# Kernel tuning notes

Measured on AMD Instinct MI355X. Metric: run time of the kernel, lower is better.

Reference implementation:

```python
import jax, jax.numpy as jnp
import numpy as np
import math

C_S = 384; C_Z = 128; C_H = 16; H = 12; PQ = 4; PV = 8; C_SURF = 16
N_RES = 512; N_SURF = 2048; B = 1
INF = 1e5; EPS = 1e-8
SOFTPLUS_INV_1 = 0.541324854612918


def _quat_to_rot(q):
    q = q / jnp.linalg.norm(q, axis=-1, keepdims=True)
    w, x, y, z = q[..., 0], q[..., 1], q[..., 2], q[..., 3]
    R = jnp.stack([
        1 - 2 * (y * y + z * z), 2 * (x * y - w * z), 2 * (x * z + w * y),
        2 * (x * y + w * z), 1 - 2 * (x * x + z * z), 2 * (y * z - w * x),
        2 * (x * z - w * y), 2 * (y * z + w * x), 1 - 2 * (x * x + y * y),
    ], axis=-1)
    return R.reshape(q.shape[:-1] + (3, 3))


def setup_inputs() -> dict:
    key = jax.random.key(0)
    ks = jax.random.split(key, 32)
    hc = H * C_H            # 192
    hpq = H * PQ * 3        # 144
    hpkv = H * (PQ + PV) * 3  # 432
    cz4 = C_Z // 4
    concat = hc + H * PV * 3 + H * PV + H * cz4 + hc  # 1152
    w = lambda k, i, o: jax.random.normal(k, (i, o), jnp.float32) * 0.02
    inp = {
        's': jax.random.normal(ks[0], (B, N_RES, C_S), jnp.float32),
        'z': jax.random.normal(ks[1], (B, N_RES, N_RES, C_Z), jnp.float32),
        'rots': _quat_to_rot(jax.random.normal(ks[2], (B, N_RES, 4), jnp.float32)),
        'trans': jax.random.normal(ks[3], (B, N_RES, 3), jnp.float32) * 10.0,
        'mask': jnp.ones((B, N_RES), jnp.float32),
        'surface_points': jax.random.normal(ks[4], (B, N_SURF, 3), jnp.float32) * 10.0,
        'surface_features': jax.random.normal(ks[5], (B, N_SURF, C_SURF), jnp.float32),
        'surface_mask': jnp.ones((B, N_SURF), jnp.float32),
        'Wq': w(ks[6], C_S, hc), 'bq': jnp.zeros((hc,)),
        'Wkv': w(ks[7], C_S, 2 * hc), 'bkv': jnp.zeros((2 * hc,)),
        'Wqp': w(ks[8], C_S, hpq), 'bqp': jnp.zeros((hpq,)),
        'Wkvp': w(ks[9], C_S, hpkv), 'bkvp': jnp.zeros((hpkv,)),
        'Wse': w(ks[10], C_SURF, C_S), 'bse': jnp.zeros((C_S,)),
        'Wsq': w(ks[11], C_S, hc), 'bsq': jnp.zeros((hc,)),
        'Wsk': w(ks[12], C_S, hc), 'bsk': jnp.zeros((hc,)),
        'Wsv': w(ks[13], C_S, hc), 'bsv': jnp.zeros((hc,)),
        'Wb': w(ks[14], C_Z, H), 'bb': jnp.zeros((H,)),
        'Wdz': w(ks[15], C_Z, cz4), 'bdz': jnp.zeros((cz4,)),
        'head_weights': jnp.full((H,), SOFTPLUS_INV_1, jnp.float32),
        'sb_weights': jnp.full((1,), SOFTPLUS_INV_1, jnp.float32),
        'Wout': w(ks[16], concat, C_S), 'bout': jnp.zeros((C_S,)),
        'Wso': w(ks[17], 2 * C_S, C_SURF), 'bso': jnp.zeros((C_SURF,)),
    }
    return inp


def reference(s, z, rots, trans, mask, surface_points, surface_features, surface_mask,
              Wq, bq, Wkv, bkv, Wqp, bqp, Wkvp, bkvp, Wse, bse, Wsq, bsq, Wsk, bsk,
              Wsv, bsv, Wb, bb, Wdz, bdz, head_weights, sb_weights, Wout, bout, Wso, bso):
    lin = lambda x, W, b: x @ W + b
    b_, n, _ = s.shape
    m = surface_points.shape[-2]

    surface_feat = lin(surface_features, Wse, bse)                    # [B,M,c_s]
    # backbone<->surface squared distances
    disp = trans[:, :, None, :] - surface_points[:, None, :, :]       # [B,N,M,3]
    dist_sq = jnp.sum(disp * disp, -1)                                # [B,N,M]

    q = lin(s, Wq, bq).reshape(b_, n, H, C_H)
    kv = lin(s, Wkv, bkv).reshape(b_, n, H, 2 * C_H)
    k, v = kv[..., :C_H], kv[..., C_H:]

    # query points: split into 3 coord chunks, stack, rigid-apply
    qp = lin(s, Wqp, bqp)
    qp = jnp.stack(jnp.split(qp, 3, axis=-1), axis=-1)                # [B,N,H*PQ,3]
    qp = jnp.einsum('bnij,bnpj->bnpi', rots, qp) + trans[:, :, None]
    qp = qp.reshape(b_, n, H, PQ, 3)

    kvp = lin(s, Wkvp, bkvp)
    kvp = jnp.stack(jnp.split(kvp, 3, axis=-1), axis=-1)              # [B,N,H*(PQ+PV),3]
    kvp = jnp.einsum('bnij,bnpj->bnpi', rots, kvp) + trans[:, :, None]
    kvp = kvp.reshape(b_, n, H, PQ + PV, 3)
    kp, vp = kvp[..., :PQ, :], kvp[..., PQ:, :]

    b_bias = lin(z, Wb, bb)                                           # [B,N,N,H]
    a = jnp.einsum('bihc,bjhc->bhij', q, k) * math.sqrt(1.0 / (3 * C_H))
    a = a + math.sqrt(1.0 / 3) * jnp.transpose(b_bias, (0, 3, 1, 2))

    # point-distance attention term
    pt = jnp.sum((qp[:, :, None] - kp[:, None]) ** 2, axis=-1)        # [B,N,N,H,PQ]
    hw = jax.nn.softplus(head_weights)                                # [H]
    pt = jnp.sum(pt, axis=-1) * hw * math.sqrt(1.0 / (3 * (PQ * 9.0 / 2))) * (-0.5)
    a = a + jnp.transpose(pt, (0, 3, 1, 2))                           # [B,H,N,N]

    sq_mask = INF * (mask[:, :, None] * mask[:, None, :] - 1.0)
    a = jax.nn.softmax(a + sq_mask[:, None], axis=-1)

    o = jnp.einsum('bhij,bjhc->bihc', a, v).reshape(b_, n, H * C_H)
    o_pt = jnp.einsum('bhij,bjhpd->bihpd', a, vp)                     # [B,N,H,PV,3]
    o_pt = jnp.einsum('bnji,bnhpj->bnhpi', rots, o_pt - trans[:, :, None, None])
    o_pt_norm = jnp.sqrt(jnp.sum(o_pt ** 2, -1) + EPS).reshape(b_, n, H * PV)
    o_pt_flat = o_pt.reshape(b_, n, H * PV, 3)

    pair_z = lin(z, Wdz, bdz)                                         # [B,N,N,cz/4]
    o_pair = jnp.einsum('bhij,bijc->bihc', a, pair_z).reshape(b_, n, -1)

    # surface cross-attention branch
    sq = lin(s, Wsq, bsq).reshape(b_, n, H, C_H)
    sk = lin(surface_feat, Wsk, bsk).reshape(b_, m, H, C_H)
    sv = lin(surface_feat, Wsv, bsv).reshape(b_, m, H, C_H)
    logits = jnp.einsum('bnhc,bmhc->bhnm', sq, sk) * math.sqrt(1.0 / C_H)
    sbw = jax.nn.softplus(sb_weights)[0]
    logits = logits - 0.5 * sbw * dist_sq[:, None]
    cross_mask = mask[:, :, None] * surface_mask[:, None, :]          # [B,N,M]
    logits = logits + INF * (cross_mask - 1.0)[:, None]
    a_s = jax.nn.softmax(logits, axis=-1)
    o_surf = jnp.einsum('bhnm,bmhc->bnhc', a_s, sv).reshape(b_, n, H * C_H)

    o_cat = jnp.concatenate([o, o_pt_flat[..., 0], o_pt_flat[..., 1], o_pt_flat[..., 2],
                             o_pt_norm, o_pair, o_surf], axis=-1)
    s_out = lin(o_cat, Wout, bout)                                    # [B,N,c_s]

    # surface update: attend surface points to backbone (softmax over residues)
    a_ts = jax.nn.softmax(jnp.swapaxes(logits, -1, -2), axis=-1).mean(axis=1)  # [B,M,N]
    s_agg = jnp.einsum('bmn,bnc->bmc', a_ts, s)
    surf_out = lin(jnp.concatenate([surface_feat, s_agg], axis=-1), Wso, bso)
    return s_out, surf_out
```

## Files before the change

### kernel.cpp

```cpp
#include <hip/hip_runtime.h>
#include <cstddef>


#define CS 384
#define INFV 100000.0f

__device__ __forceinline__ float softplusf(float x) { return log1pf(__expf(x)); }

__global__ __launch_bounds__(256) void k_pack(
    const float* __restrict__ Wq, const float* __restrict__ Wsq,
    const float* __restrict__ Wkv, const float* __restrict__ Wqp,
    const float* __restrict__ Wkvp, const float* __restrict__ Wsk,
    const float* __restrict__ Wsv, const float* __restrict__ Wout,
    const float* __restrict__ bq, const float* __restrict__ bsq,
    const float* __restrict__ bkv, const float* __restrict__ bqp,
    const float* __restrict__ bkvp, const float* __restrict__ bsk,
    const float* __restrict__ bsv,
    float* __restrict__ wt1, float* __restrict__ wt2, float* __restrict__ wt3,
    float* __restrict__ b1, float* __restrict__ b2)
{
    const int b = blockIdx.x, t = threadIdx.x;
    if (b >= 1092) {
        int idx = (b - 1092) * 256 + t;
        if (idx < 1344) {
            float v;
            if (idx < 192) v = bq[idx];
            else if (idx < 384) v = bsq[idx - 192];
            else if (idx < 768) v = bkv[idx - 384];
            else if (idx < 912) v = bqp[idx - 768];
            else v = bkvp[idx - 912];
            b1[idx] = v;
        } else if (idx < 1728) {
            int i2 = idx - 1344;
            b2[i2] = (i2 < 192) ? bsk[i2] : bsv[i2 - 192];
        }
        return;
    }
    const float* src; float* dst; int C, coff, tile, ldd;
    if (b < 72)       { src = Wq;   C = 192; dst = wt1; coff = 0;   ldd = 384;  tile = b; }
    else if (b < 144) { src = Wsq;  C = 192; dst = wt1; coff = 192; ldd = 384;  tile = b - 72; }
    else if (b < 288) { src = Wkv;  C = 384; dst = wt1; coff = 384; ldd = 384;  tile = b - 144; }
    else if (b < 348) { src = Wqp;  C = 144; dst = wt1; coff = 768; ldd = 384;  tile = b - 288; }
    else if (b < 516) { src = Wkvp; C = 432; dst = wt1; coff = 912; ldd = 384;  tile = b - 348; }
    else if (b < 588) { src = Wsk;  C = 192; dst = wt2; coff = 0;   ldd = 384;  tile = b - 516; }
    else if (b < 660) { src = Wsv;  C = 192; dst = wt2; coff = 192; ldd = 384;  tile = b - 588; }
    else              { src = Wout; C = 384; dst = wt3; coff = 0;   ldd = 1152; tile = b - 660; }
    const int cT = (C + 31) >> 5;
    const int tk = tile / cT, tc = tile % cT;
    __shared__ float l[32][33];
    const int tr = t >> 5, tcc = t & 31;
    #pragma unroll
    for (int rr = 0; rr < 4; ++rr) {
        int kloc = tr * 4 + rr;
        int cg = tc * 32 + tcc;
        l[kloc][tcc] = (cg < C) ? src[(size_t)(tk * 32 + kloc) * C + cg] : 0.f;
    }
    __syncthreads();
    #pragma unroll
    for (int rr = 0; rr < 4; ++rr) {
        int cloc = tr * 4 + rr;
        int cg = tc * 32 + cloc;
        if (cg < C) dst[(size_t)(coff + cg) * ldd + tk * 32 + tcc] = l[tcc][cloc];
    }
}

__global__ __launch_bounds__(256) void k_packz(
    const float* __restrict__ Wb, const float* __restrict__ bb,
    const float* __restrict__ Wdz, const float* __restrict__ bdz,
    float* __restrict__ wz, float* __restrict__ bz)
{
    const float s3 = 0.5773502691896258f;
    int idx = blockIdx.x * 256 + threadIdx.x;
    if (idx < 5632) {
        int c = idx >> 7, kk = idx & 127;
        wz[idx] = (c < 12) ? s3 * Wb[kk * 12 + c] : Wdz[kk * 32 + (c - 12)];
    } else if (idx < 5676) {
        int c = idx - 5632;
        bz[c] = (c < 12) ? s3 * bb[c] : bdz[c - 12];
    }
}

__global__ __launch_bounds__(256) void k_transp(
    const float* __restrict__ A, float* __restrict__ At)
{
    __shared__ float tile[32][33];
    const int r0 = blockIdx.y * 32, c0 = blockIdx.x * 32;
    const int tr = threadIdx.x >> 5, tc = threadIdx.x & 31;
    #pragma unroll
    for (int rr = 0; rr < 4; ++rr)
        tile[tr + rr * 8][tc] = A[(size_t)(r0 + tr + rr * 8) * 384 + c0 + tc];
    __syncthreads();
    #pragma unroll
    for (int rr = 0; rr < 4; ++rr)
        At[(size_t)(c0 + tr + rr * 8) * 512 + r0 + tc] = tile[tc][tr + rr * 8];
}

template<int KTOT, bool HB>
__global__ __launch_bounds__(256) void k_gemm(
    const float* __restrict__ A, const float* __restrict__ Wt,
    const float* __restrict__ bias, float* __restrict__ C, int ldc)
{
    __shared__ float As[64][68];
    __shared__ float Ws[64][68];
    const int t = threadIdx.x;
    const int c0 = blockIdx.x * 64, m0 = blockIdx.y * 64;
    const int sr = t >> 4, sk4 = (t & 15) << 2;
    const int wid = t >> 6, lane = t & 63;
    const int wr = (wid >> 1) * 32, wc = (wid & 1) * 32;
    const int lr = lane >> 3, lc = lane & 7;
    float acc[4][4];
    #pragma unroll
    for (int j = 0; j < 4; ++j) {
        float bv = HB ? bias[c0 + wc + lc + 8 * j] : 0.f;
        #pragma unroll
        for (int i = 0; i < 4; ++i) acc[i][j] = bv;
    }
    for (int kc = 0; kc < KTOT; kc += 64) {
        __syncthreads();
        #pragma unroll
        for (int rep = 0; rep < 4; ++rep) {
            int row = sr + rep * 16;
            *(float4*)&As[row][sk4] = *(const float4*)&A[(size_t)(m0 + row) * KTOT + kc + sk4];
            *(float4*)&Ws[row][sk4] = *(const float4*)&Wt[(size_t)(c0 + row) * KTOT + kc + sk4];
        }
        __syncthreads();
        #pragma unroll 4
        for (int k4 = 0; k4 < 16; ++k4) {
            float4 a[4], w[4];
            #pragma unroll
            for (int i = 0; i < 4; ++i) a[i] = *(float4*)&As[wr + lr + 8 * i][k4 * 4];
            #pragma unroll
            for (int j = 0; j < 4; ++j) w[j] = *(float4*)&Ws[wc + lc + 8 * j][k4 * 4];
            #pragma unroll
            for (int i = 0; i < 4; ++i) {
                #pragma unroll
                for (int j = 0; j < 4; ++j) {
                    acc[i][j] = fmaf(a[i].x, w[j].x, acc[i][j]);
                    acc[i][j] = fmaf(a[i].y, w[j].y, acc[i][j]);
                    acc[i][j] = fmaf(a[i].z, w[j].z, acc[i][j]);
                    acc[i][j] = fmaf(a[i].w, w[j].w, acc[i][j]);
                }
            }
        }
    }
    #pragma unroll
    for (int i = 0; i < 4; ++i) {
        #pragma unroll
        for (int j = 0; j < 4; ++j)
            C[(size_t)(m0 + wr + lr + 8 * i) * ldc + c0 + wc + lc + 8 * j] = acc[i][j];
    }
}

__global__ __launch_bounds__(256) void k_scatter(
    const float* __restrict__ proj, const float* __restrict__ rots,
    const float* __restrict__ trans,
    float* __restrict__ qw, float* __restrict__ kw, float* __restrict__ vw,
    float* __restrict__ sqw, float* __restrict__ qpw, float* __restrict__ kpw,
    float* __restrict__ vpw)
{
    __shared__ float p[4][1344];
    const int n0 = blockIdx.x * 4, t = threadIdx.x;
    for (int idx = t; idx < 1344; idx += 256) {
        #pragma unroll
        for (int r = 0; r < 4; ++r) p[r][idx] = proj[(size_t)(n0 + r) * 1344 + idx];
    }
    __syncthreads();
    for (int idx = t; idx < 3072; idx += 256) {
        int r = idx / 768, c = idx % 768;
        int n = n0 + r;
        float v = p[r][c];
        if (c < 192) qw[(size_t)n * 192 + c] = v;
        else if (c < 384) sqw[(size_t)n * 192 + (c - 192)] = v;
        else {
            int cc = c - 384, h = cc >> 5, sub = cc & 31;
            if (sub < 16) kw[(size_t)n * 192 + h * 16 + sub] = v;
            else          vw[(size_t)n * 192 + h * 16 + (sub - 16)] = v;
        }
    }
    for (int idx = t; idx < 2304; idx += 256) {
        int r = idx / 576, rem = idx % 576;
        int n = n0 + r;
        const float* R = &rots[(size_t)n * 9];
        const float* tr = &trans[(size_t)n * 3];
        if (rem < 144) {
            int pp = rem / 3, d = rem % 3;
            float v = fmaf(R[d*3+0], p[r][768 + pp],
                      fmaf(R[d*3+1], p[r][768 + 48 + pp],
                      fmaf(R[d*3+2], p[r][768 + 96 + pp], tr[d])));
            qpw[(size_t)n * 144 + pp * 3 + d] = v;
        } else {
            int rem2 = rem - 144; int pp = rem2 / 3, d = rem2 % 3;
            float v = fmaf(R[d*3+0], p[r][912 + pp],
                      fmaf(R[d*3+1], p[r][912 + 144 + pp],
                      fmaf(R[d*3+2], p[r][912 + 288 + pp], tr[d])));
            int h = pp / 12, ii = pp % 12;
            if (ii < 4) kpw[(size_t)n * 144 + h * 12 + ii * 3 + d] = v;
            else        vpw[(size_t)n * 288 + h * 24 + (ii - 4) * 3 + d] = v;
        }
    }
}

__global__ __launch_bounds__(256) void k_sfeat(
    const float* __restrict__ sf, const float* __restrict__ Wse,
    const float* __restrict__ bse, float* __restrict__ sfeat)
{
    __shared__ float wl[16 * 384];
    __shared__ float sfl[8][16];
    const int m0 = blockIdx.x * 8, t = threadIdx.x;
    for (int idx = t; idx < 6144; idx += 256) wl[idx] = Wse[idx];
    if (t < 128) sfl[t >> 4][t & 15] = sf[(size_t)(m0 + (t >> 4)) * 16 + (t & 15)];
    __syncthreads();
    #pragma unroll
    for (int u = 0; u < 12; ++u) {
        int idx = t + u * 256;
        int r = idx / 384, c = idx % 384;
        float a = bse[c];
        #pragma unroll
        for (int kk = 0; kk < 16; ++kk) a = fmaf(sfl[r][kk], wl[kk * 384 + c], a);
        sfeat[(size_t)(m0 + r) * 384 + c] = a;
    }
}

__global__ __launch_bounds__(256) void k_zpass(
    const float* __restrict__ z, const float* __restrict__ wz,
    const float* __restrict__ bz, float* __restrict__ bpz)
{
    __shared__ float zt[256][36];
    __shared__ float wt[44][32];
    const int t = threadIdx.x;
    const int jg0 = blockIdx.x * 256;
    const int i = jg0 >> 9;
    const int jloc = jg0 & 511;
    const int jl = t & 63;
    const int cgs = __builtin_amdgcn_readfirstlane(t >> 6);
    float acc[4][11];
    #pragma unroll
    for (int u = 0; u < 11; ++u) {
        float b = bz[cgs * 11 + u];
        acc[0][u] = b; acc[1][u] = b; acc[2][u] = b; acc[3][u] = b;
    }
    for (int kc = 0; kc < 128; kc += 32) {
        __syncthreads();
        for (int idx = t; idx < 352; idx += 256) {
            int c = idx >> 3, k4 = (idx & 7) << 2;
            *(float4*)&wt[c][k4] = *(const float4*)&wz[c * 128 + kc + k4];
        }
        #pragma unroll
        for (int u = 0; u < 8; ++u) {
            int idx = t + u * 256;
            int r = idx >> 3, k4 = (idx & 7) << 2;
            *(float4*)&zt[r][k4] = *(const float4*)&z[((size_t)(jg0 + r)) * 128 + kc + k4];
        }
        __syncthreads();
        const float* wbase = &wt[cgs * 11][0];
        #pragma unroll 2
        for (int k4 = 0; k4 < 32; k4 += 4) {
            float4 z0 = *(float4*)&zt[jl][k4];
            float4 z1 = *(float4*)&zt[jl + 64][k4];
            float4 z2 = *(float4*)&zt[jl + 128][k4];
            float4 z3 = *(float4*)&zt[jl + 192][k4];
            #pragma unroll
            for (int u = 0; u < 11; ++u) {
                float4 wv = *(const float4*)&wbase[u * 32 + k4];
                acc[0][u] = fmaf(z0.x, wv.x, fmaf(z0.y, wv.y,
                            fmaf(z0.z, wv.z, fmaf(z0.w, wv.w, acc[0][u]))));
                acc[1][u] = fmaf(z1.x, wv.x, fmaf(z1.y, wv.y,
                            fmaf(z1.z, wv.z, fmaf(z1.w, wv.w, acc[1][u]))));
                acc[2][u] = fmaf(z2.x, wv.x, fmaf(z2.y, wv.y,
                            fmaf(z2.z, wv.z, fmaf(z2.w, wv.w, acc[2][u]))));
                acc[3][u] = fmaf(z3.x, wv.x, fmaf(z3.y, wv.y,
                            fmaf(z3.z, wv.z, fmaf(z3.w, wv.w, acc[3][u]))));
            }
        }
    }
    #pragma unroll
    for (int u = 0; u < 11; ++u) {
        size_t base = ((size_t)i * 44 + cgs * 11 + u) * 512 + jloc;
        bpz[base + jl]       = acc[0][u];
        bpz[base + 64 + jl]  = acc[1][u];
        bpz[base + 128 + jl] = acc[2][u];
        bpz[base + 192 + jl] = acc[3][u];
    }
}

__global__ __launch_bounds__(256) void k_attn_a(
    const float* __restrict__ qw, const float* __restrict__ kw,
    const float* __restrict__ qpw, const float* __restrict__ kpw,
    const float* __restrict__ bpz, const float* __restrict__ mask,
    const float* __restrict__ hwp, float* __restrict__ abuf)
{
    __shared__ float pls[4][520];
    __shared__ float qs[64], qps[48], cpt4[4];
    const int i = blockIdx.x, hg = blockIdx.y;
    const int t = threadIdx.x;
    if (t < 64) qs[t] = qw[(size_t)i * 192 + hg * 64 + t];
    if (t < 48) qps[t] = qpw[(size_t)i * 144 + hg * 48 + t];
    if (t < 4) cpt4[t] = -0.5f * 0.13608276348795434f * softplusf(hwp[hg * 4 + t]);
    const float mask_i = mask[i];
    __syncthreads();
    #pragma unroll 2
    for (int it = 0; it < 8; ++it) {
        int idx = t + it * 256;
        int hh = idx >> 9, j = idx & 511;
        int h = hg * 4 + hh;
        float kj[16], kpj[12];
        { const float4* kr = (const float4*)&kw[(size_t)j * 192 + h * 16];
          *(float4*)&kj[0] = kr[0]; *(float4*)&kj[4] = kr[1];
          *(float4*)&kj[8] = kr[2]; *(float4*)&kj[12] = kr[3]; }
        { const float4* kr = (const float4*)&kpw[(size_t)j * 144 + h * 12];
          *(float4*)&kpj[0] = kr[0]; *(float4*)&kpj[4] = kr[1]; *(float4*)&kpj[8] = kr[2]; }
        float qk = 0.f;
        #pragma unroll
        for (int c = 0; c < 16; ++c) qk = fmaf(qs[hh * 16 + c], kj[c], qk);
        float pts = 0.f;
        #pragma unroll
        for (int p = 0; p < 4; ++p) {
            float dx = qps[hh*12+p*3+0] - kpj[p*3+0];
            float dy = qps[hh*12+p*3+1] - kpj[p*3+1];
            float dz = qps[hh*12+p*3+2] - kpj[p*3+2];
            pts += dx*dx + dy*dy + dz*dz;
        }
        float lg = fmaf(0.14433756729740643f, qk, bpz[((size_t)i * 44 + h) * 512 + j]);
        lg = fmaf(cpt4[hh], pts, lg);
        lg += INFV * (mask_i * mask[j] - 1.0f);
        pls[hh][j] = lg;
    }
    __syncthreads();
    const int w = t >> 6, lane = t & 63;
    float v[8];
    #pragma unroll
    for (int k = 0; k < 8; ++k) v[k] = pls[w][lane + k * 64];
    float mx = v[0];
    #pragma unroll
    for (int k = 1; k < 8; ++k) mx = fmaxf(mx, v[k]);
    #pragma unroll
    for (int off = 32; off; off >>= 1) mx = fmaxf(mx, __shfl_xor(mx, off));
    float sm = 0.f;
    #pragma unroll
    for (int k = 0; k < 8; ++k) { v[k] = __expf(v[k] - mx); sm += v[k]; }
    #pragma unroll
    for (int off = 32; off; off >>= 1) sm += __shfl_xor(sm, off);
    const float inv = 1.0f / sm;
    float* dst = abuf + ((size_t)(hg * 4 + w) * 512 + i) * 512;
    #pragma unroll
    for (int k = 0; k < 8; ++k) dst[lane + k * 64] = v[k] * inv;
}

__global__ __launch_bounds__(256) void k_attn_pair(
    const float* __restrict__ abuf, const float* __restrict__ bpz,
    float* __restrict__ ocat)
{
    __shared__ float al[12][512];
    const int i = blockIdx.x, t = threadIdx.x;
    #pragma unroll
    for (int u = 0; u < 12; ++u) {
        al[u][t] = abuf[(size_t)u * 262144 + (size_t)i * 512 + t];
        al[u][t + 256] = abuf[(size_t)u * 262144 + (size_t)i * 512 + t + 256];
    }
    __syncthreads();
    const int c = t & 31;
    const int h1 = t >> 5;
    const bool dual = (t < 128);
    const float* pz = bpz + ((size_t)i * 44 + 12 + c) * 512;
    const float* a1 = al[h1];
    const float* a2 = al[dual ? h1 + 8 : 0];
    float acc1 = 0.f, acc2 = 0.f;
    for (int j = 0; j < 512; j += 4) {
        float4 p = *(const float4*)&pz[j];
        acc1 = fmaf(a1[j+0], p.x, acc1);
        acc1 = fmaf(a1[j+1], p.y, acc1);
        acc1 = fmaf(a1[j+2], p.z, acc1);
        acc1 = fmaf(a1[j+3], p.w, acc1);
        if (dual) {
            acc2 = fmaf(a2[j+0], p.x, acc2);
            acc2 = fmaf(a2[j+1], p.y, acc2);
            acc2 = fmaf(a2[j+2], p.z, acc2);
            acc2 = fmaf(a2[j+3], p.w, acc2);
        }
    }
    ocat[(size_t)i * 1152 + 576 + h1 * 32 + c] = acc1;
    if (dual) ocat[(size_t)i * 1152 + 576 + (h1 + 8) * 32 + c] = acc2;
}

__global__ __launch_bounds__(256) void k_gemm_ov(
    const float* __restrict__ abuf, const float* __restrict__ vw,
    const float* __restrict__ vpw, float* __restrict__ cbuf)
{
    __shared__ float As[64][68];
    __shared__ float Bs[64][44];
    const int i0 = blockIdx.x * 64, h = blockIdx.y;
    const int t = threadIdx.x;
    const int sr = t >> 4, sk4 = (t & 15) << 2;
    const int r1 = t >> 3;
    const int cb = t & 7;
    float acc[2][5];
    #pragma unroll
    for (int u = 0; u < 5; ++u) { acc[0][u] = 0.f; acc[1][u] = 0.f; }
    for (int kc = 0; kc < 512; kc += 64) {
        __syncthreads();
        #pragma unroll
        for (int rep = 0; rep < 4; ++rep) {
            int row = sr + rep * 16;
            *(float4*)&As[row][sk4] =
                *(const float4*)&abuf[(size_t)h * 262144 + (size_t)(i0 + row) * 512 + kc + sk4];
        }
        #pragma unroll
        for (int u = 0; u < 10; ++u) {
            int idx = t + u * 256;
            int r = idx / 40, cc = idx % 40;
            Bs[r][cc] = (cc < 16) ? vw[(size_t)(kc + r) * 192 + h * 16 + cc]
                                  : vpw[(size_t)(kc + r) * 288 + h * 24 + (cc - 16)];
        }
        __syncthreads();
        #pragma unroll 4
        for (int kk = 0; kk < 64; ++kk) {
            float av1 = As[r1][kk], av2 = As[r1 + 32][kk];
            #pragma unroll
            for (int u = 0; u < 5; ++u) {
                float b = Bs[kk][cb + 8 * u];
                acc[0][u] = fmaf(av1, b, acc[0][u]);
                acc[1][u] = fmaf(av2, b, acc[1][u]);
            }
        }
    }
    #pragma unroll
    for (int u = 0; u < 5; ++u) {
        cbuf[((size_t)h * 512 + i0 + r1) * 40 + cb + 8 * u] = acc[0][u];
        cbuf[((size_t)h * 512 + i0 + r1 + 32) * 40 + cb + 8 * u] = acc[1][u];
    }
}

__global__ __launch_bounds__(256) void k_optfin(
    const float* __restrict__ cbuf, const float* __restrict__ rots,
    const float* __restrict__ trans, float* __restrict__ ocat)
{
    __shared__ float cl[4][12][40];
    const int i0 = blockIdx.x * 4, t = threadIdx.x;
    for (int idx = t; idx < 1920; idx += 256) {
        int ii = idx / 480, rem = idx % 480;
        int h = rem / 40, c = rem % 40;
        cl[ii][h][c] = cbuf[((size_t)h * 512 + i0 + ii) * 40 + c];
    }
    __syncthreads();
    for (int idx = t; idx < 768; idx += 256) {
        int ii = idx / 192, o = idx % 192;
        ocat[(size_t)(i0 + ii) * 1152 + o] = cl[ii][o >> 4][o & 15];
    }
    for (int idx = t; idx < 384; idx += 256) {
        int ii = idx / 96, hp = idx % 96;
        int h = hp >> 3, p = hp & 7;
        int i = i0 + ii;
        const float* R = &rots[(size_t)i * 9];
        float gx = cl[ii][h][16 + p*3 + 0] - trans[(size_t)i*3 + 0];
        float gy = cl[ii][h][16 + p*3 + 1] - trans[(size_t)i*3 + 1];
        float gz = cl[ii][h][16 + p*3 + 2] - trans[(size_t)i*3 + 2];
        float lx = R[0]*gx + R[3]*gy + R[6]*gz;
        float ly = R[1]*gx + R[4]*gy + R[7]*gz;
        float lz = R[2]*gx + R[5]*gy + R[8]*gz;
        float nm = sqrtf(lx*lx + ly*ly + lz*lz + 1e-8f);
        int col = h * 8 + p;
        size_t base = (size_t)i * 1152;
        ocat[base + 192 + col] = lx;
        ocat[base + 288 + col] = ly;
        ocat[base + 384 + col] = lz;
        ocat[base + 480 + col] = nm;
    }
}

__global__ __launch_bounds__(256) void k_tlog(
    const float* __restrict__ sqw, const float* __restrict__ skv,
    const float* __restrict__ trans, const float* __restrict__ mask,
    const float* __restrict__ sp, const float* __restrict__ smask,
    const float* __restrict__ sbwp, float* __restrict__ logits,
    float* __restrict__ stat_m, float* __restrict__ stat_il)
{
    __shared__ float sk_s[32][16];
    __shared__ float sq_s[32][16];
    __shared__ float trans_s[96];
    __shared__ float mask_s[32];
    __shared__ float spm_s[96];
    __shared__ float smask_s[32];
    const int h = blockIdx.y;
    const int m0 = blockIdx.x * 32;
    const int t = threadIdx.x;
    const int tmg = t >> 5, tnl = t & 31;
    const float sbw = softplusf(sbwp[0]);
    for (int idx = t; idx < 512; idx += 256) {
        int row = idx >> 4, c = idx & 15;
        sk_s[row][c] = skv[(size_t)(m0 + row) * 384 + h * 16 + c];
    }
    if (t < 96) spm_s[t] = sp[(size_t)m0 * 3 + t];
    if (t < 32) smask_s[t] = smask[m0 + t];
    __syncthreads();
    float skr[4][16];
    float spx[4], spy[4], spz[4], smk[4];
    #pragma unroll
    for (int mi = 0; mi < 4; ++mi) {
        int row = tmg * 4 + mi;
        #pragma unroll
        for (int c4 = 0; c4 < 16; c4 += 4)
            *(float4*)&skr[mi][c4] = *(float4*)&sk_s[row][c4];
        spx[mi] = spm_s[row*3+0]; spy[mi] = spm_s[row*3+1]; spz[mi] = spm_s[row*3+2];
        smk[mi] = smask_s[row];
    }
    float mxr[4], lr[4];
    #pragma unroll
    for (int mi = 0; mi < 4; ++mi) { mxr[mi] = -1e30f; lr[mi] = 0.f; }
    for (int nt = 0; nt < 16; ++nt) {
        __syncthreads();
        const int nb = nt * 32;
        if (t < 128) {
            int nn = t >> 2, c4 = (t & 3) << 2;
            *(float4*)&sq_s[nn][c4] = *(const float4*)&sqw[(size_t)(nb + nn) * 192 + h * 16 + c4];
        }
        if (t < 96) trans_s[t] = trans[(size_t)nb * 3 + t];
        if (t < 32) mask_s[t] = mask[nb + t];
        __syncthreads();
        float q[16];
        #pragma unroll
        for (int c4 = 0; c4 < 16; c4 += 4)
            *(float4*)&q[c4] = *(float4*)&sq_s[tnl][c4];
        const float tx = trans_s[tnl*3+0], ty = trans_s[tnl*3+1], tz = trans_s[tnl*3+2];
        const float mkn = mask_s[tnl];
        #pragma unroll
        for (int mi = 0; mi < 4; ++mi) {
            float dot = 0.f;
            #pragma unroll
            for (int c = 0; c < 16; ++c) dot = fmaf(skr[mi][c], q[c], dot);
            float dx = tx - spx[mi], dy = ty - spy[mi], dz = tz - spz[mi];
            float mterm = INFV * (mkn * smk[mi] - 1.0f) - 0.5f * sbw * (dx*dx + dy*dy + dz*dz);
            float lg = fmaf(0.25f, dot, mterm);
            logits[((size_t)(m0 + tmg * 4 + mi) * 12 + h) * 512 + nb + tnl] = lg;
            float newm = fmaxf(mxr[mi], lg);
            lr[mi] = lr[mi] * __expf(mxr[mi] - newm) + __expf(lg - newm);
            mxr[mi] = newm;
        }
    }
    #pragma unroll
    for (int off = 1; off < 32; off <<= 1) {
        #pragma unroll
        for (int mi = 0; mi < 4; ++mi) {
            float m2 = __shfl_xor(mxr[mi], off), l2 = __shfl_xor(lr[mi], off);
            float newm = fmaxf(mxr[mi], m2);
            lr[mi] = lr[mi] * __expf(mxr[mi] - newm) + l2 * __expf(m2 - newm);
            mxr[mi] = newm;
        }
    }
    if (tnl == 0) {
        #pragma unroll
        for (int mi = 0; mi < 4; ++mi) {
            int m = m0 + tmg * 4 + mi;
            stat_m[(size_t)m * 12 + h] = mxr[mi];
            stat_il[(size_t)m * 12 + h] = 1.0f / lr[mi];
        }
    }
}

__global__ __launch_bounds__(256) void k_rstat(
    const float* __restrict__ lbuf, float* __restrict__ rspm,
    float* __restrict__ rsps)
{
    __shared__ float smx[4][64], ssm[4][64];
    const int n0 = blockIdx.x * 64, mc = blockIdx.y, h = blockIdx.z;
    const int t = threadIdx.x, ln = t & 63, mg = t >> 6;
    const int mb = mc * 512;
    const int n = n0 + ln;
    float mx = -1e30f, sm = 0.f;
    #pragma unroll 2
    for (int it = 0; it < 128; ++it) {
        int m = mb + it * 4 + mg;
        float lg = lbuf[((size_t)m * 12 + h) * 512 + n];
        float nm = fmaxf(mx, lg);
        sm = sm * __expf(mx - nm) + __expf(lg - nm);
        mx = nm;
    }
    smx[mg][ln] = mx; ssm[mg][ln] = sm;
    __syncthreads();
    if (t < 64) {
        float M = smx[0][t], S = ssm[0][t];
        #pragma unroll
        for (int g = 1; g < 4; ++g) {
            float m2 = smx[g][t], s2 = ssm[g][t];
            float nm = fmaxf(M, m2);
            S = S * __expf(M - nm) + s2 * __expf(m2 - nm);
            M = nm;
        }
        rspm[((size_t)h * 4 + mc) * 512 + n0 + t] = M;
        rsps[((size_t)h * 4 + mc) * 512 + n0 + t] = S;
    }
}

__global__ __launch_bounds__(256) void k_rcomb(
    const float* __restrict__ rspm, const float* __restrict__ rsps,
    float* __restrict__ rmax, float* __restrict__ rinv)
{
    int gid = blockIdx.x * 256 + threadIdx.x;
    if (gid >= 6144) return;
    int h = gid >> 9, n = gid & 511;
    float M = -1e30f, S = 0.f;
    #pragma unroll
    for (int mc = 0; mc < 4; ++mc) {
        float m2 = rspm[((size_t)h * 4 + mc) * 512 + n];
        float s2 = rsps[((size_t)h * 4 + mc) * 512 + n];
        float nm = fmaxf(M, m2);
        S = S * __expf(M - nm) + s2 * __expf(m2 - nm);
        M = nm;
    }
    rmax[gid] = M;
    rinv[gid] = 1.0f / S;
}

__global__ __launch_bounds__(256) void k_pv(
    const float* __restrict__ lbuf, const float* __restrict__ skv,
    const float* __restrict__ rmax, const float* __restrict__ rinv,
    float* __restrict__ pvp)
{
    __shared__ float sv_s[512][17];
    const int n0 = blockIdx.x * 64, mc = blockIdx.y, h = blockIdx.z;
    const int t = threadIdx.x, ln = t & 63, mg = t >> 6;
    const int mb = mc * 512;
    for (int idx = t; idx < 2048; idx += 256) {
        int ml = idx >> 2, c4 = (idx & 3) << 2;
        float4 v4 = *(const float4*)&skv[(size_t)(mb + ml) * 384 + 192 + h * 16 + c4];
        sv_s[ml][c4+0]=v4.x; sv_s[ml][c4+1]=v4.y; sv_s[ml][c4+2]=v4.z; sv_s[ml][c4+3]=v4.w;
    }
    const int n = n0 + ln;
    const float rm = rmax[h * 512 + n], ri = rinv[h * 512 + n];
    float acc[16];
    #pragma unroll
    for (int c = 0; c < 16; ++c) acc[c] = 0.f;
    __syncthreads();
    #pragma unroll 2
    for (int it = 0; it < 128; ++it) {
        int ml = it * 4 + mg;
        float w = __expf(lbuf[((size_t)(mb + ml) * 12 + h) * 512 + n] - rm) * ri;
        #pragma unroll
        for (int c = 0; c < 16; ++c) acc[c] = fmaf(w, sv_s[ml][c], acc[c]);
    }
    __syncthreads();
    float* red = &sv_s[0][0];
    #pragma unroll
    for (int c = 0; c < 16; ++c) red[(mg * 64 + ln) * 17 + c] = acc[c];
    __syncthreads();
    {
        int nl = t >> 2, c4 = (t & 3) << 2;
        float4 o;
        #pragma unroll
        for (int e = 0; e < 4; ++e) {
            float s = 0.f;
            #pragma unroll
            for (int g = 0; g < 4; ++g) s += red[(g * 64 + nl) * 17 + c4 + e];
            (&o.x)[e] = s;
        }
        *(float4*)&pvp[(((size_t)h * 4 + mc) * 512 + n0 + nl) * 16 + c4] = o;
    }
}

__global__ __launch_bounds__(256) void k_pvcomb(
    const float* __restrict__ pvp, float* __restrict__ ocat)
{
    int gid = blockIdx.x * 256 + threadIdx.x;
    int n = gid / 192, rem = gid % 192;
    float o = 0.f;
    #pragma unroll
    for (int mc = 0; mc < 4; ++mc)
        o += pvp[(((size_t)(rem >> 4) * 4 + mc) * 512 + n) * 16 + (rem & 15)];
    ocat[(size_t)n * 1152 + 960 + rem] = o;
}

__global__ __launch_bounds__(256) void k_tw(
    const float* __restrict__ logits, const float* __restrict__ stat_m,
    const float* __restrict__ stat_il, float* __restrict__ w)
{
    __shared__ float mxs[12], ils[12];
    const int m = blockIdx.x, t = threadIdx.x;
    if (t < 12) { mxs[t] = stat_m[(size_t)m * 12 + t]; ils[t] = stat_il[(size_t)m * 12 + t]; }
    __syncthreads();
    const float* lp = logits + (size_t)m * 12 * 512;
    float a0 = 0.f, a1 = 0.f;
    #pragma unroll
    for (int h = 0; h < 12; ++h) {
        a0 += __expf(lp[h * 512 + t] - mxs[h]) * ils[h];
        a1 += __expf(lp[h * 512 + 256 + t] - mxs[h]) * ils[h];
    }
    w[(size_t)m * 512 + t] = a0 * (1.0f / 12.0f);
    w[(size_t)m * 512 + 256 + t] = a1 * (1.0f / 12.0f);
}

__global__ __launch_bounds__(256) void k_surf_out(
    const float* __restrict__ sfeat, const float* __restrict__ saggw,
    const float* __restrict__ Wso, const float* __restrict__ bso,
    float* __restrict__ out)
{
    __shared__ float wl[12304];
    const int t = threadIdx.x;
    for (int idx = t; idx < 12288; idx += 256) {
        int k = idx >> 4, c = idx & 15;
        wl[(k / 192) * 3076 + (k % 192) * 16 + c] = Wso[idx];
    }
    const int m = blockIdx.x * 64 + (t >> 2);
    const int kq = t & 3;
    const float* src = (kq < 2) ? &sfeat[(size_t)m * 384 + kq * 192]
                                : &saggw[(size_t)m * 384 + (kq - 2) * 192];
    __syncthreads();
    float acc[16];
    #pragma unroll
    for (int c = 0; c < 16; ++c) acc[c] = 0.f;
    const float* wb = &wl[kq * 3076];
    for (int k = 0; k < 192; k += 4) {
        float4 v = *(const float4*)&src[k];
        #pragma unroll
        for (int e = 0; e < 4; ++e) {
            float sv = (&v.x)[e];
            #pragma unroll
            for (int c = 0; c < 16; ++c)
                acc[c] = fmaf(sv, wb[(k + e) * 16 + c], acc[c]);
        }
    }
    #pragma unroll
    for (int c = 0; c < 16; ++c) {
        acc[c] += __shfl_xor(acc[c], 1);
        acc[c] += __shfl_xor(acc[c], 2);
    }
    #pragma unroll
    for (int c = 0; c < 16; ++c) {
        if ((c >> 2) == kq) out[196608 + (size_t)m * 16 + c] = acc[c] + bso[c];
    }
}

extern "C" void kernel_launch(void* const* d_in, const int* in_sizes, int n_in,
                              void* d_out, int out_size, void* d_ws, size_t ws_size,
                              hipStream_t stream)
{
    (void)in_sizes; (void)n_in; (void)out_size; (void)ws_size;
    const float* s     = (const float*)d_in[0];
    const float* z     = (const float*)d_in[1];
    const float* rots  = (const float*)d_in[2];
    const float* trans = (const float*)d_in[3];
    const float* mask  = (const float*)d_in[4];
    const float* sp    = (const float*)d_in[5];
    const float* sf    = (const float*)d_in[6];
    const float* smask = (const float*)d_in[7];
    const float* Wq    = (const float*)d_in[8];  const float* bq   = (const float*)d_in[9];
    const float* Wkv   = (const float*)d_in[10]; const float* bkv  = (const float*)d_in[11];
    const float* Wqp   = (const float*)d_in[12]; const float* bqp  = (const float*)d_in[13];
    const float* Wkvp  = (const float*)d_in[14]; const float* bkvp = (const float*)d_in[15];
    const float* Wse   = (const float*)d_in[16]; const float* bse  = (const float*)d_in[17];
    const float* Wsq   = (const float*)d_in[18]; const float* bsq  = (const float*)d_in[19];
    const float* Wsk   = (const float*)d_in[20]; const float* bsk  = (const float*)d_in[21];
    const float* Wsv   = (const float*)d_in[22]; const float* bsv  = (const float*)d_in[23];
    const float* Wb    = (const float*)d_in[24]; const float* bb   = (const float*)d_in[25];
    const float* Wdz   = (const float*)d_in[26]; const float* bdz  = (const float*)d_in[27];
    const float* hw    = (const float*)d_in[28]; const float* sbw  = (const float*)d_in[29];
    const float* Wout  = (const float*)d_in[30]; const float* bout = (const float*)d_in[31];
    const float* Wso   = (const float*)d_in[32]; const float* bso  = (const float*)d_in[33];
    float* out = (float*)d_out;

    float* qw    = (float*)d_ws;
    float* kw    = qw    + (size_t)512 * 192;
    float* vw    = kw    + (size_t)512 * 192;
    float* sqw   = vw    + (size_t)512 * 192;
    float* qpw   = sqw   + (size_t)512 * 192;
    float* kpw   = qpw   + (size_t)512 * 144;
    float* vpw   = kpw   + (size_t)512 * 144;
    float* sfeat = vpw   + (size_t)512 * 288;
    float* skv   = sfeat + (size_t)2048 * 384;
    float* ocat  = skv   + (size_t)2048 * 384;
    float* sagg  = ocat  + (size_t)512 * 1152;
    float* region = sagg + (size_t)2048 * 384;
    float* proj   = region;
    float* bpz    = region;
    float* logits = region;
    float* wt1   = region + (size_t)2048 * 12 * 512;
    float* wt2   = wt1   + (size_t)1344 * 384;
    float* wt3   = wt2   + (size_t)384 * 384;
    float* b1    = wt3   + (size_t)384 * 1152;
    float* b2    = b1    + 1344;
    float* st    = b2    + 384;
    float* wbuf  = st    + (size_t)384 * 512;
    float* statm = wbuf  + (size_t)2048 * 512;
    float* stati = statm + (size_t)2048 * 12;
    float* abuf  = stati + (size_t)2048 * 12;
    float* cbuf  = abuf  + (size_t)12 * 512 * 512;
    float* wz    = cbuf  + (size_t)12 * 512 * 40;
    float* bz    = wz    + (size_t)44 * 128;
    float* rspm  = bz    + 64;
    float* rsps  = rspm  + (size_t)12 * 4 * 512;
    float* rmax  = rsps  + (size_t)12 * 4 * 512;
    float* rinv  = rmax  + (size_t)12 * 512;
    float* pvp   = rinv  + (size_t)12 * 512;

    k_pack<<<dim3(1099), dim3(256), 0, stream>>>(Wq, Wsq, Wkv, Wqp, Wkvp, Wsk, Wsv, Wout,
        bq, bsq, bkv, bqp, bkvp, bsk, bsv, wt1, wt2, wt3, b1, b2);
    k_packz<<<dim3(23), dim3(256), 0, stream>>>(Wb, bb, Wdz, bdz, wz, bz);
    k_transp<<<dim3(12, 16), dim3(256), 0, stream>>>(s, st);
    k_gemm<384, true><<<dim3(21, 8), dim3(256), 0, stream>>>(s, wt1, b1, proj, 1344);
    k_scatter<<<dim3(128), dim3(256), 0, stream>>>(proj, rots, trans,
        qw, kw, vw, sqw, qpw, kpw, vpw);
    k_sfeat<<<dim3(256), dim3(256), 0, stream>>>(sf, Wse, bse, sfeat);
    k_gemm<384, true><<<dim3(6, 32), dim3(256), 0, stream>>>(sfeat, wt2, b2, skv, 384);
    k_zpass<<<dim3(1024), dim3(256), 0, stream>>>(z, wz, bz, bpz);
    k_attn_a<<<dim3(512, 3), dim3(256), 0, stream>>>(qw, kw, qpw, kpw, bpz, mask, hw, abuf);
    k_attn_pair<<<dim3(512), dim3(256), 0, stream>>>(abuf, bpz, ocat);
    k_gemm_ov<<<dim3(8, 12), dim3(256), 0, stream>>>(abuf, vw, vpw, cbuf);
    k_optfin<<<dim3(128), dim3(256), 0, stream>>>(cbuf, rots, trans, ocat);
    k_tlog<<<dim3(64, 12), dim3(256), 0, stream>>>(sqw, skv, trans, mask, sp, smask,
        sbw, logits, statm, stati);
    k_rstat<<<dim3(8, 4, 12), dim3(256), 0, stream>>>(logits, rspm, rsps);
    k_rcomb<<<dim3(24), dim3(256), 0, stream>>>(rspm, rsps, rmax, rinv);
    k_pv<<<dim3(8, 4, 12), dim3(256), 0, stream>>>(logits, skv, rmax, rinv, pvp);
    k_pvcomb<<<dim3(384), dim3(256), 0, stream>>>(pvp, ocat);
    k_tw<<<dim3(2048), dim3(256), 0, stream>>>(logits, statm, stati, wbuf);
    k_gemm<512, false><<<dim3(6, 32), dim3(256), 0, stream>>>(wbuf, st, nullptr, sagg, 384);
    k_surf_out<<<dim3(32), dim3(256), 0, stream>>>(sfeat, sagg, Wso, bso, out);
    k_gemm<1152, true><<<dim3(6, 8), dim3(256), 0, stream>>>(ocat, wt3, bout, out, 384);
}
```

Before: 520.4 us.

## Reformulate IPA logits as augmented dot product with online softmax stats

Adds a prep kernel that packs the scaled q, the point terms expanded as |q|^2+|k|^2-2q·k, and the mask into 32-wide augmented vectors, so each logit is a single dot product plus the pair bias. The attention kernel now tiles over 16 query rows per head, writes raw logits, and keeps an online max and sum per row. Consumers (the pair and output GEMM kernels) normalise on the fly using the stored max and inverse sum. This removes redundant per-j key loads and the separate softmax pass. In exchange it recomputes exp in two consumers and may lose some precision when expanding the squared distance.

```diff
diff --git a/kernel.cpp b/kernel.cpp
--- a/kernel.cpp
+++ b/kernel.cpp
@@ -283,79 +283,130 @@
     }
 }
 
+__global__ __launch_bounds__(256) void k_aprep(
+    const float* __restrict__ qw, const float* __restrict__ qpw,
+    const float* __restrict__ kw, const float* __restrict__ kpw,
+    const float* __restrict__ mask, const float* __restrict__ hwp,
+    float* __restrict__ aq, float* __restrict__ ak)
+{
+    __shared__ float cpt[12], sq2[12], sk2[12];
+    const int i = blockIdx.x, t = threadIdx.x;
+    if (t < 12) {
+        float c = -0.5f * 0.13608276348795434f * softplusf(hwp[t]);
+        cpt[t] = c;
+        float s = 0.f, s2 = 0.f;
+        #pragma unroll
+        for (int p = 0; p < 12; ++p) {
+            float v = qpw[(size_t)i * 144 + t * 12 + p]; s = fmaf(v, v, s);
+            float w = kpw[(size_t)i * 144 + t * 12 + p]; s2 = fmaf(w, w, s2);
+        }
+        sq2[t] = s; sk2[t] = s2;
+    }
+    __syncthreads();
+    const float mi = mask[i];
+    for (int idx = t; idx < 384; idx += 256) {
+        int h = idx >> 5, d = idx & 31;
+        float va, vb;
+        if (d < 16) {
+            va = 0.14433756729740643f * qw[(size_t)i * 192 + h * 16 + d];
+            vb = kw[(size_t)i * 192 + h * 16 + d];
+        } else if (d < 28) {
+            float qp = qpw[(size_t)i * 144 + h * 12 + (d - 16)];
+            va = -2.f * cpt[h] * qp;
+            vb = kpw[(size_t)i * 144 + h * 12 + (d - 16)];
+        } else if (d == 28) { va = cpt[h] * sq2[h]; vb = 1.f; }
+        else if (d == 29)   { va = 1.f; vb = cpt[h] * sk2[h]; }
+        else if (d == 30)   { va = mi; vb = mi; }
+        else                { va = 0.f; vb = 0.f; }
+        aq[((size_t)h * 512 + i) * 32 + d] = va;
+        ak[((size_t)h * 512 + i) * 32 + d] = vb;
+    }
+}
+
 __global__ __launch_bounds__(256) void k_attn_a(
-    const float* __restrict__ qw, const float* __restrict__ kw,
-    const float* __restrict__ qpw, const float* __restrict__ kpw,
-    const float* __restrict__ bpz, const float* __restrict__ mask,
-    const float* __restrict__ hwp, float* __restrict__ abuf)
-{
-    __shared__ float pls[4][520];
-    __shared__ float qs[64], qps[48], cpt4[4];
-    const int i = blockIdx.x, hg = blockIdx.y;
+    const float* __restrict__ aq, const float* __restrict__ ak,
+    const float* __restrict__ bpz, float* __restrict__ abuf,
+    float* __restrict__ astm, float* __restrict__ asti)
+{
+    __shared__ float aqs[16][32];
+    __shared__ float bt[32][36];
+    const int h = blockIdx.y, i0 = blockIdx.x * 16;
     const int t = threadIdx.x;
-    if (t < 64) qs[t] = qw[(size_t)i * 192 + hg * 64 + t];
-    if (t < 48) qps[t] = qpw[(size_t)i * 144 + hg * 48 + t];
-    if (t < 4) cpt4[t] = -0.5f * 0.13608276348795434f * softplusf(hwp[hg * 4 + t]);
-    const float mask_i = mask[i];
-    __syncthreads();
-    #pragma unroll 2
-    for (int it = 0; it < 8; ++it) {
-        int idx = t + it * 256;
-        int hh = idx >> 9, j = idx & 511;
-        int h = hg * 4 + hh;
-        float kj[16], kpj[12];
-        { const float4* kr = (const float4*)&kw[(size_t)j * 192 + h * 16];
-          *(float4*)&kj[0] = kr[0]; *(float4*)&kj[4] = kr[1];
-          *(float4*)&kj[8] = kr[2]; *(float4*)&kj[12] = kr[3]; }
-        { const float4* kr = (const float4*)&kpw[(size_t)j * 144 + h * 12];
-          *(float4*)&kpj[0] = kr[0]; *(float4*)&kpj[4] = kr[1]; *(float4*)&kpj[8] = kr[2]; }
-        float qk = 0.f;
-        #pragma unroll
-        for (int c = 0; c < 16; ++c) qk = fmaf(qs[hh * 16 + c], kj[c], qk);
-        float pts = 0.f;
-        #pragma unroll
-        for (int p = 0; p < 4; ++p) {
-            float dx = qps[hh*12+p*3+0] - kpj[p*3+0];
-            float dy = qps[hh*12+p*3+1] - kpj[p*3+1];
-            float dz = qps[hh*12+p*3+2] - kpj[p*3+2];
-            pts += dx*dx + dy*dy + dz*dz;
-        }
-        float lg = fmaf(0.14433756729740643f, qk, bpz[((size_t)i * 44 + h) * 512 + j]);
-        lg = fmaf(cpt4[hh], pts, lg);
-        lg += INFV * (mask_i * mask[j] - 1.0f);
-        pls[hh][j] = lg;
-    }
-    __syncthreads();
-    const int w = t >> 6, lane = t & 63;
-    float v[8];
-    #pragma unroll
-    for (int k = 0; k < 8; ++k) v[k] = pls[w][lane + k * 64];
-    float mx = v[0];
-    #pragma unroll
-    for (int k = 1; k < 8; ++k) mx = fmaxf(mx, v[k]);
-    #pragma unroll
-    for (int off = 32; off; off >>= 1) mx = fmaxf(mx, __shfl_xor(mx, off));
-    float sm = 0.f;
-    #pragma unroll
-    for (int k = 0; k < 8; ++k) { v[k] = __expf(v[k] - mx); sm += v[k]; }
-    #pragma unroll
-    for (int off = 32; off; off >>= 1) sm += __shfl_xor(sm, off);
-    const float inv = 1.0f / sm;
-    float* dst = abuf + ((size_t)(hg * 4 + w) * 512 + i) * 512;
-    #pragma unroll
-    for (int k = 0; k < 8; ++k) dst[lane + k * 64] = v[k] * inv;
+    const int ig = t >> 5, tnl = t & 31;
+    if (t < 128)
+        *(float4*)&aqs[t >> 3][(t & 7) << 2] =
+            *(const float4*)&aq[((size_t)h * 512 + i0 + (t >> 3)) * 32 + ((t & 7) << 2)];
+    __syncthreads();
+    float ar[2][32];
+    #pragma unroll
+    for (int r = 0; r < 2; ++r)
+        #pragma unroll
+        for (int d4 = 0; d4 < 32; d4 += 4)
+            *(float4*)&ar[r][d4] = *(float4*)&aqs[ig * 2 + r][d4];
+    float mx[2] = {-1e30f, -1e30f}, sm[2] = {0.f, 0.f};
+    for (int jt = 0; jt < 16; ++jt) {
+        __syncthreads();
+        {
+            int r = t >> 3, d4 = (t & 7) << 2;
+            *(float4*)&bt[r][d4] =
+                *(const float4*)&ak[((size_t)h * 512 + jt * 32 + r) * 32 + d4];
+        }
+        __syncthreads();
+        const int j = jt * 32 + tnl;
+        float br[32];
+        #pragma unroll
+        for (int d4 = 0; d4 < 32; d4 += 4)
+            *(float4*)&br[d4] = *(float4*)&bt[tnl][d4];
+        #pragma unroll
+        for (int r = 0; r < 2; ++r) {
+            const int i = i0 + ig * 2 + r;
+            float dot = 0.f;
+            #pragma unroll
+            for (int d = 0; d < 30; ++d) dot = fmaf(ar[r][d], br[d], dot);
+            float lg = dot + bpz[((size_t)i * 44 + h) * 512 + j];
+            lg += INFV * (ar[r][30] * br[30] - 1.0f);
+            abuf[((size_t)h * 512 + i) * 512 + j] = lg;
+            float nm = fmaxf(mx[r], lg);
+            sm[r] = sm[r] * __expf(mx[r] - nm) + __expf(lg - nm);
+            mx[r] = nm;
+        }
+    }
+    #pragma unroll
+    for (int off = 1; off < 32; off <<= 1) {
+        #pragma unroll
+        for (int r = 0; r < 2; ++r) {
+            float m2 = __shfl_xor(mx[r], off), s2 = __shfl_xor(sm[r], off);
+            float nm = fmaxf(mx[r], m2);
+            sm[r] = sm[r] * __expf(mx[r] - nm) + s2 * __expf(m2 - nm);
+            mx[r] = nm;
+        }
+    }
+    if (tnl == 0) {
+        #pragma unroll
+        for (int r = 0; r < 2; ++r) {
+            int i = i0 + ig * 2 + r;
+            astm[(size_t)h * 512 + i] = mx[r];
+            asti[(size_t)h * 512 + i] = 1.0f / sm[r];
+        }
+    }
 }
 
 __global__ __launch_bounds__(256) void k_attn_pair(
     const float* __restrict__ abuf, const float* __restrict__ bpz,
+    const float* __restrict__ astm, const float* __restrict__ asti,
     float* __restrict__ ocat)
 {
     __shared__ float al[12][512];
+    __shared__ float mh[12], ih[12];
     const int i = blockIdx.x, t = threadIdx.x;
+    if (t < 12) { mh[t] = astm[(size_t)t * 512 + i]; ih[t] = asti[(size_t)t * 512 + i]; }
+    __syncthreads();
     #pragma unroll
     for (int u = 0; u < 12; ++u) {
-        al[u][t] = abuf[(size_t)u * 262144 + (size_t)i * 512 + t];
-        al[u][t + 256] = abuf[(size_t)u * 262144 + (size_t)i * 512 + t + 256];
+        float r0 = abuf[(size_t)u * 262144 + (size_t)i * 512 + t];
+        float r1 = abuf[(size_t)u * 262144 + (size_t)i * 512 + t + 256];
+        al[u][t] = __expf(r0 - mh[u]) * ih[u];
+        al[u][t + 256] = __expf(r1 - mh[u]) * ih[u];
     }
     __syncthreads();
     const int c = t & 31;
@@ -384,15 +435,21 @@
 
 __global__ __launch_bounds__(256) void k_gemm_ov(
     const float* __restrict__ abuf, const float* __restrict__ vw,
-    const float* __restrict__ vpw, float* __restrict__ cbuf)
+    const float* __restrict__ vpw, const float* __restrict__ astm,
+    const float* __restrict__ asti, float* __restrict__ cbuf)
 {
     __shared__ float As[64][68];
     __shared__ float Bs[64][44];
+    __shared__ float ms[64], is_[64];
     const int i0 = blockIdx.x * 64, h = blockIdx.y;
     const int t = threadIdx.x;
     const int sr = t >> 4, sk4 = (t & 15) << 2;
     const int r1 = t >> 3;
     const int cb = t & 7;
+    if (t < 64) {
+        ms[t] = astm[(size_t)h * 512 + i0 + t];
+        is_[t] = asti[(size_t)h * 512 + i0 + t];
+    }
     float acc[2][5];
     #pragma unroll
     for (int u = 0; u < 5; ++u) { acc[0][u] = 0.f; acc[1][u] = 0.f; }
@@ -401,8 +458,15 @@
         #pragma unroll
         for (int rep = 0; rep < 4; ++rep) {
             int row = sr + rep * 16;
-            *(float4*)&As[row][sk4] =
-                *(const float4*)&abuf[(size_t)h * 262144 + (size_t)(i0 + row) * 512 + kc + sk4];
+            float4 raw = *(const float4*)&abuf[(size_t)h * 262144 +
+                                               (size_t)(i0 + row) * 512 + kc + sk4];
+            float m = ms[row], iv = is_[row];
+            float4 w;
+            w.x = __expf(raw.x - m) * iv;
+            w.y = __expf(raw.y - m) * iv;
+            w.z = __expf(raw.z - m) * iv;
+            w.w = __expf(raw.w - m) * iv;
+            *(float4*)&As[row][sk4] = w;
         }
         #pragma unroll
         for (int u = 0; u < 10; ++u) {
@@ -789,6 +853,10 @@
     float* rmax  = rsps  + (size_t)12 * 4 * 512;
     float* rinv  = rmax  + (size_t)12 * 512;
     float* pvp   = rinv  + (size_t)12 * 512;
+    float* aq    = pvp   + (size_t)12 * 4 * 512 * 16;
+    float* ak    = aq    + (size_t)12 * 512 * 32;
+    float* astm  = ak    + (size_t)12 * 512 * 32;
+    float* asti  = astm  + (size_t)12 * 512;
 
     k_pack<<<dim3(1099), dim3(256), 0, stream>>>(Wq, Wsq, Wkv, Wqp, Wkvp, Wsk, Wsv, Wout,
         bq, bsq, bkv, bqp, bkvp, bsk, bsv, wt1, wt2, wt3, b1, b2);
@@ -797,12 +865,13 @@
     k_gemm<384, true><<<dim3(21, 8), dim3(256), 0, stream>>>(s, wt1, b1, proj, 1344);
     k_scatter<<<dim3(128), dim3(256), 0, stream>>>(proj, rots, trans,
         qw, kw, vw, sqw, qpw, kpw, vpw);
+    k_aprep<<<dim3(512), dim3(256), 0, stream>>>(qw, qpw, kw, kpw, mask, hw, aq, ak);
     k_sfeat<<<dim3(256), dim3(256), 0, stream>>>(sf, Wse, bse, sfeat);
     k_gemm<384, true><<<dim3(6, 32), dim3(256), 0, stream>>>(sfeat, wt2, b2, skv, 384);
     k_zpass<<<dim3(1024), dim3(256), 0, stream>>>(z, wz, bz, bpz);
-    k_attn_a<<<dim3(512, 3), dim3(256), 0, stream>>>(qw, kw, qpw, kpw, bpz, mask, hw, abuf);
-    k_attn_pair<<<dim3(512), dim3(256), 0, stream>>>(abuf, bpz, ocat);
-    k_gemm_ov<<<dim3(8, 12), dim3(256), 0, stream>>>(abuf, vw, vpw, cbuf);
+    k_attn_a<<<dim3(32, 12), dim3(256), 0, stream>>>(aq, ak, bpz, abuf, astm, asti);
+    k_attn_pair<<<dim3(512), dim3(256), 0, stream>>>(abuf, bpz, astm, asti, ocat);
+    k_gemm_ov<<<dim3(8, 12), dim3(256), 0, stream>>>(abuf, vw, vpw, astm, asti, cbuf);
     k_optfin<<<dim3(128), dim3(256), 0, stream>>>(cbuf, rots, trans, ocat);
     k_tlog<<<dim3(64, 12), dim3(256), 0, stream>>>(sqw, skv, trans, mask, sp, smask,
         sbw, logits, statm, stati);
```

Result: faster. 467.6 us, median of 2 (-10.1%).
